# Kernel tuning notes

Hardware: AMD Instinct MI355X
Metric: run time of the kernel (lower is better)

The kernel has to match this reference:

```python
import jax, jax.numpy as jnp
import numpy as np

B, T, N, D, R, K, P = 4, 336, 862, 64, 8, 6, 96


def setup_inputs() -> dict:
    key = jax.random.key(0)
    ks = jax.random.split(key, 8)
    s = 0.02
    return {
        "x_enc": jax.random.normal(ks[0], (B, T, N), jnp.float32),
        "W_embed": jax.random.normal(ks[1], (1, D), jnp.float32) * s,
        "b_embed": jnp.zeros((D,), jnp.float32),
        "W1": jax.random.normal(ks[2], (D, R), jnp.float32) * s,
        "W2": jax.random.normal(ks[3], (D, R), jnp.float32) * s,
        "gate": jnp.float32(-4.0),  # gate_init
        "A_prior": jnp.eye(N, dtype=jnp.float32),  # season_gcn_adj_source=identity
        "W_gcn": jax.random.normal(ks[4], (D, D), jnp.float32) * s,
        "g_gcn": jnp.float32(0.5),  # season_gcn gate
        "W_head": jax.random.normal(ks[5], (T * D, P), jnp.float32) * s,
        "b_head": jnp.zeros((P,), jnp.float32),
    }


def _topk_renorm(adj, k):
    # keep top-k entries per row, zero the rest, renormalize rows (matches _sparsify_adj)
    vals = jax.lax.top_k(adj, k)[0]
    thresh = vals[..., -1:]
    mask = (adj >= thresh).astype(adj.dtype)
    masked = adj * mask
    denom = jnp.clip(jnp.sum(masked, axis=-1, keepdims=True), 1e-12, None)
    return masked / denom


def reference(x_enc, W_embed, b_embed, W1, W2, gate, A_prior, W_gcn, g_gcn, W_head, b_head):
    # per-variable, per-timestep value embedding: [B,N,T,D]
    h = x_enc.transpose(0, 2, 1)[..., None] * W_embed[0] + b_embed
    # content-mean node descriptors: [B,N,D]
    z = jnp.mean(h, axis=2)
    # low-rank graph learner -> adjacency logits [B,N,N]
    e1 = z @ W1
    e2 = z @ W2
    logits = jnp.einsum('bnr,bmr->bnm', e1, e2) / jnp.sqrt(jnp.float32(R))
    adj = jax.nn.softmax(logits, axis=-1)
    adj = _topk_renorm(adj, K)  # top-k sparsify + row renorm
    # gated graph mixing over variable nodes
    h_mix = jnp.einsum('bnm,bmtd->bntd', adj, h)
    h = h + jax.nn.sigmoid(gate) * h_mix
    # season GCN: sym-normalized prior adjacency, residual + gate
    deg = jnp.sum(A_prior, axis=-1)
    dinv = jnp.where(deg > 0, 1.0 / jnp.sqrt(deg), 0.0)
    A_hat = A_prior * dinv[:, None] * dinv[None, :]
    h = h + g_gcn * jnp.einsum('nm,bmtd,de->bnte', A_hat, h, W_gcn)
    # forecast head: flatten tokens, project to pred_len per variable
    out = h.reshape(B, N, T * D) @ W_head + b_head  # [B,N,P]
    return out.transpose(0, 2, 1)  # [B,P,N]
```

## Files before the change

### kernel.cpp

```cpp
#include <hip/hip_runtime.h>
#include <math.h>

#define B_ 4
#define T_ 336
#define N_ 862
#define D_ 64
#define R_ 8
#define K_ 6
#define P_ 96
#define NR 896
#define CAP 32
#define NB 864

#define OFF_PCQ  0
#define OFF_XBP  768
#define OFF_DINV 21504
#define OFF_WGT  22368
#define OFF_IDX  43104
#define OFF_CNT  63840
#define OFF_CSRV 64704
#define OFF_CSRI 92352
#define OFF_P12  120000
#define OFF_PCP  184512
#define OFF_XPT  249024

__global__ __launch_bounds__(192) void kA_prep(const float* __restrict__ x,
                                               const float* __restrict__ Whead,
                                               const float* __restrict__ A,
                                               const float* __restrict__ We,
                                               const float* __restrict__ be,
                                               const float* __restrict__ gate,
                                               const float* __restrict__ Wgcn,
                                               float* __restrict__ ws) {
  int id = blockIdx.x;
  int tid = threadIdx.x;
  if (id < 336) {
    __shared__ float swh[6144];
    __shared__ float sW1[64], sW2[64], sCB[64], sWe[64];
    int t = id;
    const float* wbase = Whead + (size_t)t * (D_ * P_);
#pragma unroll
    for (int s = 0; s < 8; ++s) {
      int idx4 = s * 192 + tid;
      *(float4*)(swh + idx4 * 4) = *(const float4*)(wbase + idx4 * 4);
    }
    float g = 1.f / (1.f + expf(-gate[0]));
    if (tid < 64) {
      float a = 0.f;
#pragma unroll
      for (int dd = 0; dd < D_; ++dd) a += We[dd] * Wgcn[dd * D_ + tid];
      sW1[tid] = a;
    } else if (tid < 128) {
      int e = tid - 64;
      float a = 0.f;
#pragma unroll
      for (int dd = 0; dd < D_; ++dd) a += be[dd] * Wgcn[dd * D_ + e];
      sW2[e] = (1.f + g) * a;
    } else {
      int e = tid - 128;
      sCB[e] = (1.f + g) * be[e];
      sWe[e] = We[e];
    }
    __syncthreads();
    int c = tid, p = c % P_, sel = c / P_;
    const float* cA = sel ? sW1 : sWe;
    const float* cB = sel ? sW2 : sCB;
    float a = 0.f, bacc = 0.f;
#pragma unroll
    for (int e = 0; e < D_; ++e) {
      float w = swh[e * P_ + p];
      a = fmaf(cA[e], w, a);
      bacc = fmaf(cB[e], w, bacc);
    }
    ws[OFF_P12 + t * 192 + c] = a;
    ws[OFF_PCP + t * 192 + c] = bacc;
  } else if (id < 672) {
    __shared__ float part[192];
    int iq = id - 336;
    int b = iq / 84, rem = iq % 84;
    int ch = rem / 6, tg = rem % 6;
    int lane = tid & 63, tsub = tid >> 6;
    int n = ch * 64 + lane;
    float s = 0.f;
    if (n < N_) {
      const float* xp = x + (size_t)(b * T_) * N_ + n;
      int tend = tg * 56 + 56;
#pragma unroll 4
      for (int t = tg * 56 + tsub; t < tend; t += 3) s += xp[(size_t)t * N_];
    }
    part[tid] = s;
    __syncthreads();
    if (tsub == 0 && n < N_)
      ws[OFF_XBP + (size_t)(b * 6 + tg) * NB + n] =
          part[lane] + part[64 + lane] + part[128 + lane];
  } else {
    int lane = tid & 63, wv = tid >> 6;
    int n = (id - 672) * 3 + wv;
    if (n >= N_) return;
    const float* ap = A + (size_t)n * N_;
    float* vout = ws + OFF_CSRV;
    int* iout = (int*)(ws + OFF_CSRI);
    float s = 0.f;
    int total = 0;
    for (int base = 0; base < N_; base += 64) {
      int m = base + lane;
      float a = (m < N_) ? ap[m] : 0.f;
      s += a;
      bool nz = (a != 0.f);
      unsigned long long mask = __ballot(nz);
      int pos = __popcll(mask & ((1ull << lane) - 1ull));
      if (nz) {
        int slot = total + pos;
        if (slot < CAP) { vout[slot * NB + n] = a; iout[slot * NB + n] = m; }
      }
      total += __popcll(mask);
    }
    for (int off = 32; off; off >>= 1) s += __shfl_down(s, off);
    if (lane == 0) {
      ws[OFF_DINV + n] = (s > 0.f) ? (1.f / sqrtf(s)) : 0.f;
      ((int*)(ws + OFF_CNT))[n] = (total <= CAP) ? total : -1;
    }
  }
}

__global__ __launch_bounds__(256) void kM_mid(const float* __restrict__ x,
                                              const float* __restrict__ W1,
                                              const float* __restrict__ W2,
                                              const float* __restrict__ We,
                                              const float* __restrict__ be,
                                              const float* __restrict__ gate,
                                              float* __restrict__ ws) {
  __shared__ float smem[9600];
  int id = blockIdx.x;
  int tid = threadIdx.x;
  if (id < 432) {
    float* xs = smem;
    float* ps = smem + 384;
    int b = id / 108;
    int n0 = (id % 108) * 8;
    int cg_ = tid & 63, ng = tid >> 6;
    int c0 = cg_ * 3;
    const float* P = ws + OFF_P12;
    float a00 = 0.f, a01 = 0.f, a10 = 0.f, a11 = 0.f, a20 = 0.f, a21 = 0.f;
    for (int kc = 0; kc < 7; ++kc) {
      int t0 = kc * 48;
      if (tid < 96) {
        int row = tid >> 1, col4 = (tid & 1) * 4;
        const float* xr = x + (size_t)(b * T_ + t0 + row) * N_;
        if (n0 + 7 < N_) {
          *(float4*)(xs + row * 8 + col4) = *(const float4*)(xr + n0 + col4);
        } else {
          float* dst = xs + row * 8 + col4;
#pragma unroll
          for (int q = 0; q < 4; ++q) {
            int nn = n0 + col4 + q; if (nn > N_ - 1) nn = N_ - 1;
            dst[q] = xr[nn];
          }
        }
      }
#pragma unroll
      for (int sIdx = 0; sIdx < 9; ++sIdx) {
        int i4 = tid + sIdx * 256;
        int row = i4 / 48, col4 = i4 % 48;
        *(float4*)(ps + row * 192 + col4 * 4) =
            *(const float4*)(P + (size_t)(t0 + row) * 192 + col4 * 4);
      }
      __syncthreads();
#pragma unroll 6
      for (int kk = 0; kk < 48; ++kk) {
        float x0 = xs[kk * 8 + ng * 2];
        float x1 = xs[kk * 8 + ng * 2 + 1];
        float p0 = ps[kk * 192 + c0];
        float p1 = ps[kk * 192 + c0 + 1];
        float p2 = ps[kk * 192 + c0 + 2];
        a00 = fmaf(p0, x0, a00); a01 = fmaf(p0, x1, a01);
        a10 = fmaf(p1, x0, a10); a11 = fmaf(p1, x1, a11);
        a20 = fmaf(p2, x0, a20); a21 = fmaf(p2, x1, a21);
      }
      __syncthreads();
    }
    int n = n0 + ng * 2;
    float accs[3][2] = {{a00, a01}, {a10, a11}, {a20, a21}};
#pragma unroll
    for (int cc = 0; cc < 3; ++cc) {
      float* op = ws + OFF_XPT + ((size_t)(b * 192 + c0 + cc)) * NR + n;
      if (n + 1 < N_) { *(float2*)op = *(float2*)accs[cc]; }
      else if (n < N_) { op[0] = accs[cc][0]; }
    }
  } else if (id < 436) {
    __shared__ float s_sc[4][R_];
    __shared__ float s_scal[5];
    __shared__ float selv[12];
    __shared__ int seli[12];
    float* sx = smem;
    float* wkmax = smem + 864;
    float* wkmin = smem + 1728;
    int b = id - 432;
    if (tid < 16) {
      int r = tid & 7, which = tid >> 3;
      const float* W = which ? W2 : W1;
      float a = 0.f, bb = 0.f;
      for (int dd = 0; dd < D_; ++dd) {
        float w = W[dd * R_ + r];
        a += We[dd] * w; bb += be[dd] * w;
      }
      s_sc[which * 2][r] = a; s_sc[which * 2 + 1][r] = bb;
    }
    const float invT = 1.f / (float)T_;
    for (int i = tid; i < NB; i += 256) {
      float v = 0.f;
      if (i < N_) {
        const float* xp = ws + OFF_XBP + (size_t)(b * 6) * NB + i;
#pragma unroll
        for (int q = 0; q < 6; ++q) v += xp[q * NB];
        v *= invT;
      }
      sx[i] = v;
      wkmax[i] = (i < N_) ? v : -3.4e38f;
      wkmin[i] = (i < N_) ? v : 3.4e38f;
    }
    __syncthreads();
    if (tid == 0) {
      float s11 = 0.f, s12 = 0.f, s21 = 0.f, s22 = 0.f;
      for (int r = 0; r < R_; ++r) {
        s11 += s_sc[0][r] * s_sc[2][r];
        s12 += s_sc[0][r] * s_sc[3][r];
        s21 += s_sc[1][r] * s_sc[2][r];
        s22 += s_sc[1][r] * s_sc[3][r];
      }
      s_scal[0] = s11; s_scal[1] = s12; s_scal[2] = s21; s_scal[3] = s22;
      s_scal[4] = 1.f / (1.f + expf(-gate[0]));
    }
    if (tid < 64) {
      int lane = tid;
      for (int r = 0; r < K_; ++r) {
        float bv = -3.4e38f; int bi = 0;
        for (int i = lane; i < N_; i += 64) {
          float v = wkmax[i];
          if (v > bv) { bv = v; bi = i; }
        }
        for (int off = 32; off; off >>= 1) {
          float ov = __shfl_down(bv, off);
          int oi = __shfl_down(bi, off);
          if (ov > bv) { bv = ov; bi = oi; }
        }
        bv = __shfl(bv, 0); bi = __shfl(bi, 0);
        if (lane == 0) { selv[r] = bv; seli[r] = bi; wkmax[bi] = -3.4e38f; }
      }
    } else if (tid < 128) {
      int lane = tid - 64;
      for (int r = 0; r < K_; ++r) {
        float bv = 3.4e38f; int bi = 0;
        for (int i = lane; i < N_; i += 64) {
          float v = wkmin[i];
          if (v < bv) { bv = v; bi = i; }
        }
        for (int off = 32; off; off >>= 1) {
          float ov = __shfl_down(bv, off);
          int oi = __shfl_down(bi, off);
          if (ov < bv) { bv = ov; bi = oi; }
        }
        bv = __shfl(bv, 0); bi = __shfl(bi, 0);
        if (lane == 0) { selv[6 + r] = bv; seli[6 + r] = bi; wkmin[bi] = 3.4e38f; }
      }
    }
    __syncthreads();
    float s11 = s_scal[0], s12 = s_scal[1], s21 = s_scal[2], s22 = s_scal[3];
    float g = s_scal[4];
    const float rsq = 0.3535533906f;
    for (int n = tid; n < N_; n += 256) {
      float xn = sx[n];
      float alpha = (xn * s11 + s21) * rsq;
      float beta  = (xn * s12 + s22) * rsq;
      int base = (alpha >= 0.f) ? 0 : 6;
      float l[K_]; float mx = -3.4e38f;
#pragma unroll
      for (int j = 0; j < K_; ++j) { l[j] = alpha * selv[base + j] + beta; mx = fmaxf(mx, l[j]); }
      float e[K_]; float ss = 0.f;
#pragma unroll
      for (int j = 0; j < K_; ++j) { e[j] = expf(l[j] - mx); ss += e[j]; }
      float sc = g / ss;
#pragma unroll
      for (int j = 0; j < K_; ++j) {
        ws[OFF_WGT + j * (4 * NB) + b * NB + n] = e[j] * sc;
        ((int*)(ws + OFF_IDX))[j * (4 * NB) + b * NB + n] = seli[base + j];
      }
    }
  } else {
    int q = id - 436;
    if (tid < 192) {
      float s = 0.f;
#pragma unroll 12
      for (int t = q * 84; t < q * 84 + 84; ++t) s += ws[OFF_PCP + t * 192 + tid];
      ws[OFF_PCQ + q * 192 + tid] = s;
    }
  }
}

__global__ __launch_bounds__(256) void kF_final(const float* __restrict__ A,
                                                const float* __restrict__ bhead,
                                                const float* __restrict__ ggcn,
                                                const float* __restrict__ ws,
                                                float* __restrict__ out) {
  int c = blockIdx.y;
  int n = blockIdx.x * 256 + threadIdx.x;
  if (n >= N_) return;
  int b = c / P_, p = c % P_;
  const float* Xp1 = ws + OFF_XPT + ((size_t)(b * 192 + p)) * NR;
  const float* Xp2 = ws + OFF_XPT + ((size_t)(b * 192 + P_ + p)) * NR;
  const float* WGTb = ws + OFF_WGT + b * NB;
  const int* IDXb = (const int*)(ws + OFF_IDX) + b * NB;
  float gg = ggcn[0];
  float PCp = 0.f, PAp = 0.f;
#pragma unroll
  for (int q = 0; q < 4; ++q) {
    PCp += ws[OFF_PCQ + q * 192 + p];
    PAp += ws[OFF_PCQ + q * 192 + 96 + p];
  }
  float wj[K_]; int ij[K_];
#pragma unroll
  for (int j = 0; j < K_; ++j) {
    wj[j] = WGTb[j * (4 * NB) + n];
    ij[j] = IDXb[j * (4 * NB) + n];
  }
  float acc1 = Xp1[n];
#pragma unroll
  for (int j = 0; j < K_; ++j) acc1 += wj[j] * Xp1[ij[j]];
  int cnt = ((const int*)(ws + OFF_CNT))[n];
  float S = 0.f;
  if (cnt >= 0) {
    const float* vv = ws + OFF_CSRV;
    const int* ii = (const int*)(ws + OFF_CSRI);
    for (int jj = 0; jj < cnt; ++jj) {
      float a = vv[jj * NB + n];
      int m = ii[jj * NB + n];
      float mix2 = Xp2[m];
      if (m == n) {
#pragma unroll
        for (int j = 0; j < K_; ++j) mix2 += wj[j] * Xp2[ij[j]];
      } else {
#pragma unroll
        for (int j = 0; j < K_; ++j)
          mix2 += WGTb[j * (4 * NB) + m] * Xp2[IDXb[j * (4 * NB) + m]];
      }
      S += a * ws[OFF_DINV + m] * (mix2 + PAp);
    }
  } else {
    const float* ar = A + (size_t)n * N_;
    for (int m = 0; m < N_; ++m) {
      float a = ar[m];
      if (a != 0.f) {
        float mix2 = Xp2[m];
#pragma unroll
        for (int j = 0; j < K_; ++j)
          mix2 += WGTb[j * (4 * NB) + m] * Xp2[IDXb[j * (4 * NB) + m]];
        S += a * ws[OFF_DINV + m] * (mix2 + PAp);
      }
    }
  }
  out[(size_t)c * N_ + n] = acc1 + gg * ws[OFF_DINV + n] * S + PCp + bhead[p];
}

extern "C" void kernel_launch(void* const* d_in, const int* in_sizes, int n_in,
                              void* d_out, int out_size, void* d_ws, size_t ws_size,
                              hipStream_t stream) {
  const float* x     = (const float*)d_in[0];
  const float* We    = (const float*)d_in[1];
  const float* be    = (const float*)d_in[2];
  const float* W1    = (const float*)d_in[3];
  const float* W2    = (const float*)d_in[4];
  const float* gate  = (const float*)d_in[5];
  const float* A     = (const float*)d_in[6];
  const float* Wgcn  = (const float*)d_in[7];
  const float* ggcn  = (const float*)d_in[8];
  const float* Whead = (const float*)d_in[9];
  const float* bhead = (const float*)d_in[10];
  float* ws = (float*)d_ws;
  float* out = (float*)d_out;

  kA_prep<<<960, 192, 0, stream>>>(x, Whead, A, We, be, gate, Wgcn, ws);
  kM_mid<<<440, 256, 0, stream>>>(x, W1, W2, We, be, gate, ws);
  kF_final<<<dim3(4, 384), 256, 0, stream>>>(A, bhead, ggcn, ws, out);
}
```

Measured before the change: 115.4 us.

## Retile mid-stage projection GEMM and read W_head directly from global

The projection GEMM in kM_mid is retiled. Each block now covers 16 nodes and half of the 192 output columns, using 192 threads that each compute a 4x2 tile, with float4 shared-memory loads of the projection slice. The per-block shared footprint drops, so more blocks can fit per CU. Separately, kA_prep no longer stages W_head in shared memory and instead reads it per thread straight from global memory, which is coalesced across p. The launch width and the tail loops of the other branches are adjusted to 192 threads, so the graph-learner blocks now run with fewer threads.

After: 109.4 us. 5.2% less time.

```diff
diff --git a/kernel.cpp b/kernel.cpp
--- a/kernel.cpp
+++ b/kernel.cpp
@@ -35,15 +35,8 @@
   int id = blockIdx.x;
   int tid = threadIdx.x;
   if (id < 336) {
-    __shared__ float swh[6144];
     __shared__ float sW1[64], sW2[64], sCB[64], sWe[64];
     int t = id;
-    const float* wbase = Whead + (size_t)t * (D_ * P_);
-#pragma unroll
-    for (int s = 0; s < 8; ++s) {
-      int idx4 = s * 192 + tid;
-      *(float4*)(swh + idx4 * 4) = *(const float4*)(wbase + idx4 * 4);
-    }
     float g = 1.f / (1.f + expf(-gate[0]));
     if (tid < 64) {
       float a = 0.f;
@@ -65,10 +58,11 @@
     int c = tid, p = c % P_, sel = c / P_;
     const float* cA = sel ? sW1 : sWe;
     const float* cB = sel ? sW2 : sCB;
+    const float* wrow = Whead + (size_t)t * D_ * P_ + p;
     float a = 0.f, bacc = 0.f;
 #pragma unroll
     for (int e = 0; e < D_; ++e) {
-      float w = swh[e * P_ + p];
+      float w = wrow[(size_t)e * P_];
       a = fmaf(cA[e], w, a);
       bacc = fmaf(cB[e], w, bacc);
     }
@@ -123,69 +117,71 @@
   }
 }
 
-__global__ __launch_bounds__(256) void kM_mid(const float* __restrict__ x,
+__global__ __launch_bounds__(192) void kM_mid(const float* __restrict__ x,
                                               const float* __restrict__ W1,
                                               const float* __restrict__ W2,
                                               const float* __restrict__ We,
                                               const float* __restrict__ be,
                                               const float* __restrict__ gate,
                                               float* __restrict__ ws) {
-  __shared__ float smem[9600];
+  __shared__ float smem[5376];
   int id = blockIdx.x;
   int tid = threadIdx.x;
   if (id < 432) {
     float* xs = smem;
-    float* ps = smem + 384;
+    float* ps = smem + 768;
     int b = id / 108;
-    int n0 = (id % 108) * 8;
-    int cg_ = tid & 63, ng = tid >> 6;
-    int c0 = cg_ * 3;
+    int rem = id % 108;
+    int n0 = (rem >> 1) * 16;
+    int ch = (rem & 1) * 96;
+    int cq = tid % 24, nq = tid / 24;
+    int c0 = cq * 4;
     const float* P = ws + OFF_P12;
-    float a00 = 0.f, a01 = 0.f, a10 = 0.f, a11 = 0.f, a20 = 0.f, a21 = 0.f;
+    float acc[4][2];
+#pragma unroll
+    for (int i = 0; i < 4; ++i) { acc[i][0] = 0.f; acc[i][1] = 0.f; }
+    int xrow = tid >> 2, xcol4 = tid & 3;
     for (int kc = 0; kc < 7; ++kc) {
       int t0 = kc * 48;
-      if (tid < 96) {
-        int row = tid >> 1, col4 = (tid & 1) * 4;
-        const float* xr = x + (size_t)(b * T_ + t0 + row) * N_;
-        if (n0 + 7 < N_) {
-          *(float4*)(xs + row * 8 + col4) = *(const float4*)(xr + n0 + col4);
+      {
+        const float* xr = x + (size_t)(b * T_ + t0 + xrow) * N_;
+        if (n0 + 15 < N_) {
+          *(float4*)(xs + xrow * 16 + xcol4 * 4) = *(const float4*)(xr + n0 + xcol4 * 4);
         } else {
-          float* dst = xs + row * 8 + col4;
+          float* dst = xs + xrow * 16 + xcol4 * 4;
 #pragma unroll
           for (int q = 0; q < 4; ++q) {
-            int nn = n0 + col4 + q; if (nn > N_ - 1) nn = N_ - 1;
+            int nn = n0 + xcol4 * 4 + q; if (nn > N_ - 1) nn = N_ - 1;
             dst[q] = xr[nn];
           }
         }
       }
 #pragma unroll
-      for (int sIdx = 0; sIdx < 9; ++sIdx) {
-        int i4 = tid + sIdx * 256;
-        int row = i4 / 48, col4 = i4 % 48;
-        *(float4*)(ps + row * 192 + col4 * 4) =
-            *(const float4*)(P + (size_t)(t0 + row) * 192 + col4 * 4);
+      for (int sIdx = 0; sIdx < 6; ++sIdx) {
+        int i4 = tid + sIdx * 192;
+        int row = i4 / 24, col4 = i4 % 24;
+        *(float4*)(ps + row * 96 + col4 * 4) =
+            *(const float4*)(P + (size_t)(t0 + row) * 192 + ch + col4 * 4);
       }
       __syncthreads();
 #pragma unroll 6
       for (int kk = 0; kk < 48; ++kk) {
-        float x0 = xs[kk * 8 + ng * 2];
-        float x1 = xs[kk * 8 + ng * 2 + 1];
-        float p0 = ps[kk * 192 + c0];
-        float p1 = ps[kk * 192 + c0 + 1];
-        float p2 = ps[kk * 192 + c0 + 2];
-        a00 = fmaf(p0, x0, a00); a01 = fmaf(p0, x1, a01);
-        a10 = fmaf(p1, x0, a10); a11 = fmaf(p1, x1, a11);
-        a20 = fmaf(p2, x0, a20); a21 = fmaf(p2, x1, a21);
+        float x0 = xs[kk * 16 + nq * 2];
+        float x1 = xs[kk * 16 + nq * 2 + 1];
+        float4 pv = *(const float4*)(ps + kk * 96 + c0);
+        acc[0][0] = fmaf(pv.x, x0, acc[0][0]); acc[0][1] = fmaf(pv.x, x1, acc[0][1]);
+        acc[1][0] = fmaf(pv.y, x0, acc[1][0]); acc[1][1] = fmaf(pv.y, x1, acc[1][1]);
+        acc[2][0] = fmaf(pv.z, x0, acc[2][0]); acc[2][1] = fmaf(pv.z, x1, acc[2][1]);
+        acc[3][0] = fmaf(pv.w, x0, acc[3][0]); acc[3][1] = fmaf(pv.w, x1, acc[3][1]);
       }
       __syncthreads();
     }
-    int n = n0 + ng * 2;
-    float accs[3][2] = {{a00, a01}, {a10, a11}, {a20, a21}};
-#pragma unroll
-    for (int cc = 0; cc < 3; ++cc) {
-      float* op = ws + OFF_XPT + ((size_t)(b * 192 + c0 + cc)) * NR + n;
-      if (n + 1 < N_) { *(float2*)op = *(float2*)accs[cc]; }
-      else if (n < N_) { op[0] = accs[cc][0]; }
+    int n = n0 + nq * 2;
+#pragma unroll
+    for (int cc = 0; cc < 4; ++cc) {
+      float* op = ws + OFF_XPT + ((size_t)(b * 192 + ch + c0 + cc)) * NR + n;
+      if (n + 1 < N_) { float2 v; v.x = acc[cc][0]; v.y = acc[cc][1]; *(float2*)op = v; }
+      else if (n < N_) { op[0] = acc[cc][0]; }
     }
   } else if (id < 436) {
     __shared__ float s_sc[4][R_];
@@ -207,7 +203,7 @@
       s_sc[which * 2][r] = a; s_sc[which * 2 + 1][r] = bb;
     }
     const float invT = 1.f / (float)T_;
-    for (int i = tid; i < NB; i += 256) {
+    for (int i = tid; i < NB; i += 192) {
       float v = 0.f;
       if (i < N_) {
         const float* xp = ws + OFF_XBP + (size_t)(b * 6) * NB + i;
@@ -268,7 +264,7 @@
     float s11 = s_scal[0], s12 = s_scal[1], s21 = s_scal[2], s22 = s_scal[3];
     float g = s_scal[4];
     const float rsq = 0.3535533906f;
-    for (int n = tid; n < N_; n += 256) {
+    for (int n = tid; n < N_; n += 192) {
       float xn = sx[n];
       float alpha = (xn * s11 + s21) * rsq;
       float beta  = (xn * s12 + s22) * rsq;
@@ -379,6 +375,6 @@
   float* out = (float*)d_out;
 
   kA_prep<<<960, 192, 0, stream>>>(x, Whead, A, We, be, gate, Wgcn, ws);
-  kM_mid<<<440, 256, 0, stream>>>(x, W1, W2, We, be, gate, ws);
+  kM_mid<<<440, 192, 0, stream>>>(x, W1, W2, We, be, gate, ws);
   kF_final<<<dim3(4, 384), 256, 0, stream>>>(A, bhead, ggcn, ws, out);
 }
```
